# Kernel optimization log

Hardware: AMD Instinct MI355X
Metric: run time of the kernel (lower is better)

Reference implementation:

```python
import jax, jax.numpy as jnp
import numpy as np

N, E, D, F, T, P, C = 100000, 50000, 128, 128, 128, 128, 256


def sparsemax(z):
    """Sparsemax along the last axis (Martins & Astudillo 2016)."""
    K = z.shape[-1]
    zs = -jnp.sort(-z, axis=-1)  # descending
    k = jnp.arange(1, K + 1, dtype=z.dtype)
    zc = jnp.cumsum(zs, axis=-1)
    support = (1.0 + k * zs) > zc
    kz = jnp.sum(support, axis=-1, keepdims=True).astype(z.dtype)
    tau = (jnp.sum(jnp.where(support, zs, 0.0), axis=-1, keepdims=True) - 1.0) / kz
    return jnp.maximum(z - tau, 0.0)


def time_encode(dt, w, b):
    return jnp.cos(dt[:, None] * w[None, :] + b[None, :])


def gru_update(msg, h, W_ih, b_ih, W_hh, b_hh):
    gi = msg @ W_ih.T + b_ih  # [M,3D]
    gh = h @ W_hh.T + b_hh
    r = jax.nn.sigmoid(gi[:, :D] + gh[:, :D])
    z = jax.nn.sigmoid(gi[:, D:2 * D] + gh[:, D:2 * D])
    n = jnp.tanh(gi[:, 2 * D:] + r * gh[:, 2 * D:])
    return (1.0 - z) * n + z * h


def setup_inputs() -> dict:
    key = jax.random.key(0)
    ks = jax.random.split(key, 16)
    s = 0.05
    return {
        'node_memory': jax.random.normal(ks[0], (N, D), jnp.float32),
        'last_update': jax.random.uniform(ks[1], (N,), jnp.float32),
        'node_features': jax.random.normal(ks[2], (N, D), jnp.float32),
        'event_feat': jax.random.normal(ks[3], (E, F), jnp.float32),
        't': jax.random.uniform(ks[4], (E,), jnp.float32) * 10.0,
        'src': jax.random.randint(ks[5], (E,), 0, N),
        'dst': jax.random.randint(ks[6], (E,), 0, N),
        'time_w': jax.random.normal(ks[7], (T,), jnp.float32),
        'time_b': jax.random.normal(ks[8], (T,), jnp.float32),
        'W_ih': jax.random.normal(ks[9], (3 * D, 2 * D + F + T), jnp.float32) * s,
        'b_ih': jnp.zeros((3 * D,), jnp.float32),
        'W_hh': jax.random.normal(ks[10], (3 * D, D), jnp.float32) * s,
        'b_hh': jnp.zeros((3 * D,), jnp.float32),
        'proj_W': jax.random.normal(ks[11], (D, P), jnp.float32) * s,
        'proj_b': jnp.zeros((P,), jnp.float32),
        'centroids': jax.random.normal(ks[12], (C, P), jnp.float32),
    }


def reference(node_memory, last_update, node_features, event_feat, t, src, dst,
              time_w, time_b, W_ih, b_ih, W_hh, b_hh, proj_W, proj_b, centroids):
    # --- store_events: original events + flipped direction (sn + dn stores) ---
    idx = jnp.concatenate([src, dst])            # [2E] destination-of-update node
    other = jnp.concatenate([dst, src])          # [2E]
    tt = jnp.concatenate([t, t])                 # [2E]
    ef = jnp.concatenate([event_feat, event_feat])  # [2E,F]

    # --- message function: concat(self-mem, other-mem, event-feat, time-enc) ---
    dt = tt - last_update[idx]
    msg = jnp.concatenate([node_memory[idx], node_memory[other], ef,
                           time_encode(dt, time_w, time_b)], axis=-1)  # [2E, 2D+F+T]

    # --- message aggregator (mean) + scatter_max of timestamps ---
    msg_sum = jax.ops.segment_sum(msg, idx, num_segments=N)
    cnt = jax.ops.segment_sum(jnp.ones_like(tt), idx, num_segments=N)
    agg = msg_sum / jnp.maximum(cnt, 1.0)[:, None]
    has = cnt > 0
    upd_t = jax.ops.segment_max(tt, idx, num_segments=N)

    # --- memory updater (GRU) applied only where events arrived ---
    upd_memory = gru_update(agg, node_memory, W_ih, b_ih, W_hh, b_hh)
    new_memory = jnp.where(has[:, None], upd_memory, node_memory)  # [N,D]
    new_last = jnp.where(has, jnp.maximum(upd_t, last_update), last_update)

    # --- _detect_communities ---
    feat = new_memory + node_features
    pf = feat @ proj_W + proj_b  # [N,P]
    pf_n = pf / (jnp.linalg.norm(pf, axis=-1, keepdims=True) + 1e-8)
    cen_n = centroids / (jnp.linalg.norm(centroids, axis=-1, keepdims=True) + 1e-8)
    sim = pf_n @ cen_n.T                     # [N,C] cosine similarity
    nc_membership = sparsemax(sim)           # [N,C]
    cn_membership = sparsemax(sim.T)         # [C,N]
    c_memory = cn_membership @ new_memory    # [C,D]
    # community last-update via masked max (scatter_max over nonzero memberships)
    c_t = jnp.max(jnp.where(cn_membership > 0, new_last[None, :], -jnp.inf), axis=1)

    # --- embedder readout: node memory enriched with community memory ---
    emb = new_memory + nc_membership @ c_memory  # [N,D]
    return emb
```

## Files before the change

kernel.cpp:

```cpp
#include <hip/hip_runtime.h>
#include <math.h>

#define N_NODES 100000
#define N_EV    50000
#define CAP     6144
#define MAXE    24

typedef __attribute__((ext_vector_type(8))) short short8;
typedef __attribute__((ext_vector_type(4))) float f32x4;
typedef __attribute__((ext_vector_type(8))) _Float16 half8;

static __device__ __forceinline__ short f2bf(float f) {
    union { float f; unsigned u; } v; v.f = f;
    unsigned r = (v.u + 0x7FFFu + ((v.u >> 16) & 1u)) >> 16;
    return (short)r;
}
static __device__ __forceinline__ float bf2f(short h) {
    union { unsigned u; float f; } v; v.u = ((unsigned)(unsigned short)h) << 16;
    return v.f;
}
static __device__ __forceinline__ float fast_cos(float x) {
    float r = x * 0.15915494309189535f;
    r = r - floorf(r);
    return __builtin_amdgcn_cosf(r);
}
static __device__ __forceinline__ float fast_sigmoid(float x) {
    float e = __builtin_amdgcn_exp2f(-1.4426950408889634f * x);
    return __builtin_amdgcn_rcpf(1.f + e);
}
static __device__ __forceinline__ float fast_tanh(float x) {
    float e = __builtin_amdgcn_exp2f(2.8853900817779268f * x);
    return 1.f - 2.f * __builtin_amdgcn_rcpf(e + 1.f);
}

__global__ void k_build(const float* __restrict__ W_ih, const float* __restrict__ b_ih,
                        const float* __restrict__ W_hh, const float* __restrict__ b_hh,
                        short* __restrict__ Wbf, float* __restrict__ bcat) {
    int idx = blockIdx.x * 256 + threadIdx.x;
    int j = idx & 7, lane = (idx >> 3) & 63, sub = idx >> 9;
    int ks = sub & 15, NB = sub >> 4;
    int k = ks * 32 + ((lane >> 4) & 3) * 8 + j;
    int o = NB * 16 + (lane & 15);
    int g = o >> 7, d = o & 127;
    float v;
    if (g == 0)      v = W_ih[d * 512 + k] + (k < 128 ? W_hh[d * 128 + k] : 0.f);
    else if (g == 1) v = W_ih[(128 + d) * 512 + k] + (k < 128 ? W_hh[(128 + d) * 128 + k] : 0.f);
    else if (g == 2) v = W_ih[(256 + d) * 512 + k];
    else             v = (k < 128 ? W_hh[(256 + d) * 128 + k] : 0.f);
    Wbf[idx] = f2bf(v);
    if (idx < 512) {
        int gg = idx >> 7, dd = idx & 127;
        float b;
        if (gg == 0)      b = b_ih[dd] + b_hh[dd];
        else if (gg == 1) b = b_ih[128 + dd] + b_hh[128 + dd];
        else if (gg == 2) b = b_ih[256 + dd];
        else              b = b_hh[256 + dd];
        bcat[idx] = b;
    }
}

__global__ void k_cen(const float* __restrict__ centroids,
                      short* __restrict__ cenf_hi, short* __restrict__ cenf_lo) {
    int c = blockIdx.x, t = threadIdx.x;
    float v = centroids[c * 128 + t];
    float ss = v * v;
    #pragma unroll
    for (int m = 1; m < 64; m <<= 1) ss += __shfl_xor(ss, m);
    __shared__ float tmp[2];
    if ((t & 63) == 0) tmp[t >> 6] = ss;
    __syncthreads();
    float tot = tmp[0] + tmp[1];
    float nv = v / (sqrtf(tot) + 1e-8f);
    short hi = f2bf(nv);
    short lo = f2bf(nv - bf2f(hi));
    int ct = c >> 4, c_l = c & 15, kstep = t >> 5, kj = t & 31;
    int lane = c_l + 16 * (kj >> 3), j = kj & 7;
    int fidx = ((ct * 4 + kstep) * 64 + lane) * 8 + j;
    cenf_hi[fidx] = hi;
    cenf_lo[fidx] = lo;
}

__global__ void k_packW(const float* __restrict__ proj_W,
                        short* __restrict__ pw_hi, short* __restrict__ pw_lo) {
    int idx = blockIdx.x * 256 + threadIdx.x;
    int k = idx >> 7, p = idx & 127;
    float v = proj_W[k * 128 + p];
    short hi = f2bf(v);
    short lo = f2bf(v - bf2f(hi));
    int pt = p >> 4, p_l = p & 15, kstep = k >> 5, kj = k & 31;
    int lane = p_l + 16 * (kj >> 3), j = kj & 7;
    int fidx = ((pt * 4 + kstep) * 64 + lane) * 8 + j;
    pw_hi[fidx] = hi;
    pw_lo[fidx] = lo;
}

__global__ __launch_bounds__(256) void k_fill(
        const float* __restrict__ t_arr, const int* __restrict__ src,
        const int* __restrict__ dst, int* __restrict__ cnt_i,
        int4* __restrict__ elist) {
    int e = blockIdx.x * 256 + threadIdx.x;
    if (e >= 2 * N_EV) return;
    int eb  = e < N_EV ? e : e - N_EV;
    int idx = e < N_EV ? src[eb] : dst[eb];
    int oth = e < N_EV ? dst[eb] : src[eb];
    float tt = t_arr[eb];
    int p = atomicAdd(&cnt_i[idx], 1);
    if (p < MAXE)
        elist[(size_t)idx * MAXE + p] = make_int4(eb, oth, __float_as_int(tt), 0);
}

__global__ __launch_bounds__(512, 4) void k_gru(
        const float* __restrict__ node_memory, const float* __restrict__ last_update,
        const float* __restrict__ event_feat,
        const float* __restrict__ time_w, const float* __restrict__ time_b,
        const int* __restrict__ cnt_i, const int4* __restrict__ elist,
        const short* __restrict__ Wbf, const float* __restrict__ bcat,
        float* __restrict__ new_mem) {
    __shared__ __align__(16) short Ab[32 * 512];
    int t = threadIdx.x;
    int n0 = blockIdx.x * 32;
    int g = t >> 4, q = t & 15;
    int n = n0 + g;
    int rawc = cnt_i[n];
    int ec = rawc < MAXE ? rawc : MAXE;
    float lu = last_update[n];
    float tw[8], tb[8];
    #pragma unroll
    for (int j = 0; j < 8; j++) { tw[j] = time_w[q * 8 + j]; tb[j] = time_b[q * 8 + j]; }
    float ao[8], af[8], at[8];
    #pragma unroll
    for (int j = 0; j < 8; j++) { ao[j] = 0.f; af[j] = 0.f; at[j] = 0.f; }
    const int4* ep = elist + (size_t)n * MAXE;
    #pragma unroll
    for (int e = 0; e < 4; e++) {
        if (e < ec) {
            int4 ev = ep[e];
            int eb = ev.x, oth = ev.y;
            float dt = __int_as_float(ev.z) - lu;
            const float4* om = (const float4*)&node_memory[(size_t)oth * 128 + q * 8];
            const float4* ef = (const float4*)&event_feat[(size_t)eb * 128 + q * 8];
            float4 o0 = om[0], o1 = om[1];
            float4 f0 = ef[0], f1 = ef[1];
            ao[0] += o0.x; ao[1] += o0.y; ao[2] += o0.z; ao[3] += o0.w;
            ao[4] += o1.x; ao[5] += o1.y; ao[6] += o1.z; ao[7] += o1.w;
            af[0] += f0.x; af[1] += f0.y; af[2] += f0.z; af[3] += f0.w;
            af[4] += f1.x; af[5] += f1.y; af[6] += f1.z; af[7] += f1.w;
            #pragma unroll
            for (int j = 0; j < 8; j++) at[j] += fast_cos(fmaf(dt, tw[j], tb[j]));
        }
    }
    for (int e = 4; e < ec; e++) {
        int4 ev = ep[e];
        int eb = ev.x, oth = ev.y;
        float dt = __int_as_float(ev.z) - lu;
        const float4* om = (const float4*)&node_memory[(size_t)oth * 128 + q * 8];
        const float4* ef = (const float4*)&event_feat[(size_t)eb * 128 + q * 8];
        float4 o0 = om[0], o1 = om[1];
        float4 f0 = ef[0], f1 = ef[1];
        ao[0] += o0.x; ao[1] += o0.y; ao[2] += o0.z; ao[3] += o0.w;
        ao[4] += o1.x; ao[5] += o1.y; ao[6] += o1.z; ao[7] += o1.w;
        af[0] += f0.x; af[1] += f0.y; af[2] += f0.z; af[3] += f0.w;
        af[4] += f1.x; af[5] += f1.y; af[6] += f1.z; af[7] += f1.w;
        #pragma unroll
        for (int j = 0; j < 8; j++) at[j] += fast_cos(fmaf(dt, tw[j], tb[j]));
    }
    float inv = 1.f / fmaxf((float)rawc, 1.f);
    #pragma unroll
    for (int pass = 0; pass < 4; pass++) {
        float vals[8];
        if (pass == 0) {
            const float4* p = (const float4*)&node_memory[(size_t)n * 128 + q * 8];
            float4 x = p[0], y = p[1];
            vals[0]=x.x; vals[1]=x.y; vals[2]=x.z; vals[3]=x.w;
            vals[4]=y.x; vals[5]=y.y; vals[6]=y.z; vals[7]=y.w;
        } else if (pass == 1) {
            #pragma unroll
            for (int j = 0; j < 8; j++) vals[j] = ao[j] * inv;
        } else if (pass == 2) {
            #pragma unroll
            for (int j = 0; j < 8; j++) vals[j] = af[j] * inv;
        } else {
            #pragma unroll
            for (int j = 0; j < 8; j++) vals[j] = at[j] * inv;
        }
        int k0 = q * 8 + pass * 128;
        int mb = g >> 4, ks = k0 >> 5;
        int lane = ((k0 >> 3) & 3) * 16 + (g & 15);
        int gi = (mb * 16 + ks) * 64 + lane;
        gi ^= ((gi >> 4) & 7);
        short8 sv;
        #pragma unroll
        for (int j = 0; j < 8; j++) sv[j] = f2bf(vals[j]);
        *(short8*)&Ab[gi * 8] = sv;
    }
    __syncthreads();

    int w = t >> 6, l = t & 63;
    f32x4 acc[2][4];
    #pragma unroll
    for (int mb = 0; mb < 2; mb++)
        #pragma unroll
        for (int gg = 0; gg < 4; gg++) acc[mb][gg] = (f32x4){0.f, 0.f, 0.f, 0.f};

    const short8* Bp = (const short8*)Wbf;
    #pragma unroll 4
    for (int ks = 0; ks < 16; ks++) {
        short8 afr[2];
        #pragma unroll
        for (int mb = 0; mb < 2; mb++) {
            int gi = (mb * 16 + ks) * 64 + l;
            gi ^= ((gi >> 4) & 7);
            afr[mb] = *(const short8*)&Ab[gi * 8];
        }
        #pragma unroll
        for (int gate = 0; gate < 4; gate++) {
            short8 bfr = Bp[(((w + 8 * gate) * 16 + ks) * 64) + l];
            acc[0][gate] = __builtin_amdgcn_mfma_f32_16x16x32_bf16(afr[0], bfr, acc[0][gate], 0, 0, 0);
            acc[1][gate] = __builtin_amdgcn_mfma_f32_16x16x32_bf16(afr[1], bfr, acc[1][gate], 0, 0, 0);
        }
    }

    int c_l = l & 15, rq = l >> 4;
    int d = w * 16 + c_l;
    float br = bcat[d], bz = bcat[128 + d], bn = bcat[256 + d], bh = bcat[384 + d];
    #pragma unroll
    for (int mb = 0; mb < 2; mb++)
        #pragma unroll
        for (int r = 0; r < 4; r++) {
            int nn = n0 + mb * 16 + rq * 4 + r;
            int cn = cnt_i[nn];
            float h = node_memory[(size_t)nn * 128 + d];
            float rs = acc[mb][0][r] + br;
            float zs = acc[mb][1][r] + bz;
            float gn = acc[mb][2][r] + bn;
            float gh = acc[mb][3][r] + bh;
            float r_ = fast_sigmoid(rs);
            float z_ = fast_sigmoid(zs);
            float nn2 = fast_tanh(gn + r_ * gh);
            float nm = (1.f - z_) * nn2 + z_ * h;
            new_mem[(size_t)nn * 128 + d] = (cn > 0) ? nm : h;
        }
}

__global__ __launch_bounds__(256, 2) void k_sim(
        const float* __restrict__ new_mem, const float* __restrict__ node_features,
        const short* __restrict__ pw_hi, const short* __restrict__ pw_lo,
        const float* __restrict__ proj_b,
        const short* __restrict__ cenf_hi, const short* __restrict__ cenf_lo,
        _Float16* __restrict__ simT) {
    __shared__ __align__(16) float feat[64 * 128];
    __shared__ __align__(16) short pfh[64 * 128];
    __shared__ __align__(16) short pfl[64 * 128];
    int t = threadIdx.x;
    int n0 = blockIdx.x * 64;

    #pragma unroll
    for (int r = 0; r < 8; r++) {
        int idx = r * 256 + t;
        int node = idx >> 5, gk = idx & 31;
        float4 v = make_float4(0.f, 0.f, 0.f, 0.f);
        int n = n0 + node;
        if (n < N_NODES) {
            float4 a = *(const float4*)&new_mem[(size_t)n * 128 + gk * 4];
            float4 b = *(const float4*)&node_features[(size_t)n * 128 + gk * 4];
            v = make_float4(a.x + b.x, a.y + b.y, a.z + b.z, a.w + b.w);
        }
        int gs = gk ^ (node & 7);
        *(float4*)&feat[(node * 32 + gs) * 4] = v;
    }
    __syncthreads();

    int w = t >> 6, l = t & 63;
    int lm = l & 15, lk = l >> 4;

    f32x4 pacc[8];
    #pragma unroll
    for (int nb = 0; nb < 8; nb++) pacc[nb] = (f32x4){0.f, 0.f, 0.f, 0.f};
    #pragma unroll
    for (int ks = 0; ks < 4; ks++) {
        int node = w * 16 + lm;
        int gk0 = ks * 8 + lk * 2;
        float4 a0 = *(const float4*)&feat[(node * 32 + (gk0 ^ (node & 7))) * 4];
        float4 a1 = *(const float4*)&feat[(node * 32 + ((gk0 + 1) ^ (node & 7))) * 4];
        float av[8] = {a0.x, a0.y, a0.z, a0.w, a1.x, a1.y, a1.z, a1.w};
        short8 Ah, Al;
        #pragma unroll
        for (int j = 0; j < 8; j++) {
            short h = f2bf(av[j]);
            Ah[j] = h;
            Al[j] = f2bf(av[j] - bf2f(h));
        }
        #pragma unroll
        for (int nb = 0; nb < 8; nb++) {
            int fidx = ((nb * 4 + ks) * 64 + l) * 8;
            short8 Bh = *(const short8*)&pw_hi[fidx];
            short8 Bl = *(const short8*)&pw_lo[fidx];
            pacc[nb] = __builtin_amdgcn_mfma_f32_16x16x32_bf16(Ah, Bh, pacc[nb], 0, 0, 0);
            pacc[nb] = __builtin_amdgcn_mfma_f32_16x16x32_bf16(Ah, Bl, pacc[nb], 0, 0, 0);
            pacc[nb] = __builtin_amdgcn_mfma_f32_16x16x32_bf16(Al, Bh, pacc[nb], 0, 0, 0);
        }
    }
    float ssq[4] = {0.f, 0.f, 0.f, 0.f};
    #pragma unroll
    for (int nb = 0; nb < 8; nb++) {
        float pb = proj_b[nb * 16 + lm];
        #pragma unroll
        for (int r = 0; r < 4; r++) {
            pacc[nb][r] += pb;
            ssq[r] = fmaf(pacc[nb][r], pacc[nb][r], ssq[r]);
        }
    }
    #pragma unroll
    for (int m = 1; m < 16; m <<= 1)
        #pragma unroll
        for (int r = 0; r < 4; r++) ssq[r] += __shfl_xor(ssq[r], m);
    float inv[4];
    #pragma unroll
    for (int r = 0; r < 4; r++) inv[r] = 1.f / (sqrtf(ssq[r]) + 1e-8f);
    #pragma unroll
    for (int nb = 0; nb < 8; nb++)
        #pragma unroll
        for (int r = 0; r < 4; r++) {
            float v = pacc[nb][r] * inv[r];
            short h = f2bf(v);
            short lo2 = f2bf(v - bf2f(h));
            int node = w * 16 + lk * 4 + r;
            int p = nb * 16 + lm;
            int g = node * 16 + (((p >> 3)) ^ (node & 7));
            int si = g * 8 + (p & 7);
            pfh[si] = h;
            pfl[si] = lo2;
        }
    __syncthreads();

    f32x4 sacc[4][4];
    #pragma unroll
    for (int ct = 0; ct < 4; ct++)
        #pragma unroll
        for (int mt = 0; mt < 4; mt++) sacc[ct][mt] = (f32x4){0.f, 0.f, 0.f, 0.f};
    #pragma unroll
    for (int ks = 0; ks < 4; ks++) {
        short8 Bh[4], Bl[4];
        #pragma unroll
        for (int mt = 0; mt < 4; mt++) {
            int node = mt * 16 + lm;
            int g = node * 16 + ((ks * 4 + lk) ^ (node & 7));
            Bh[mt] = *(const short8*)&pfh[g * 8];
            Bl[mt] = *(const short8*)&pfl[g * 8];
        }
        #pragma unroll
        for (int ct = 0; ct < 4; ct++) {
            int ctg = w * 4 + ct;
            int fidx = ((ctg * 4 + ks) * 64 + l) * 8;
            short8 Ah = *(const short8*)&cenf_hi[fidx];
            short8 Al = *(const short8*)&cenf_lo[fidx];
            #pragma unroll
            for (int mt = 0; mt < 4; mt++) {
                sacc[ct][mt] = __builtin_amdgcn_mfma_f32_16x16x32_bf16(Ah, Bh[mt], sacc[ct][mt], 0, 0, 0);
                sacc[ct][mt] = __builtin_amdgcn_mfma_f32_16x16x32_bf16(Ah, Bl[mt], sacc[ct][mt], 0, 0, 0);
                sacc[ct][mt] = __builtin_amdgcn_mfma_f32_16x16x32_bf16(Al, Bh[mt], sacc[ct][mt], 0, 0, 0);
            }
        }
    }
    #pragma unroll
    for (int ct = 0; ct < 4; ct++) {
        int cbase = (w * 4 + ct) * 16 + lk * 4;
        #pragma unroll
        for (int r = 0; r < 4; r++) {
            size_t rowoff = (size_t)(cbase + r) * N_NODES;
            #pragma unroll
            for (int mt = 0; mt < 4; mt++) {
                int n = n0 + mt * 16 + lm;
                if (n < N_NODES) simT[rowoff + n] = (_Float16)sacc[ct][mt][r];
            }
        }
    }
}

static __device__ float tau_eval(const float* __restrict__ g, int cid, float lo, float w) {
    float K[32], S[32];
    #pragma unroll
    for (int j = 0; j < 32; j++)
        K[j] = g[cid * 128 + j] + g[cid * 128 + 32 + j] + g[cid * 128 + 64 + j] + g[cid * 128 + 96 + j];
    float acc = 0.f;
    for (int b = 31; b >= 0; b--) {
        float Kn = (b == 31) ? 0.f : K[b + 1];
        acc += (K[b] - Kn) * (lo + b * w);
        S[b] = acc;
    }
    float tau = (S[0] - 1.f) / fmaxf(K[0], 1.f);
    float best = tau;
    int jprev = -1;
    for (int it = 0; it < 48; it++) {
        int j = (int)floorf((tau - lo) / w);
        j = j < 0 ? 0 : (j > 31 ? 31 : j);
        if (j > 0 && lo + j * w > tau) j--;
        float Kj = K[j];
        if (Kj < 0.5f) break;
        float tn = (S[j] - 1.f) / Kj;
        if (tn > best) best = tn;
        if (j == jprev) break;
        jprev = j;
        tau = tn;
    }
    return best;
}

template <int LVL>
__global__ __launch_bounds__(256) void k_lad(const _Float16* __restrict__ simT,
                                             const float* __restrict__ g0,
                                             float* __restrict__ gout) {
    constexpr float W = (LVL == 0) ? 0.0625f : 0.008f;
    int cid = blockIdx.x >> 2, slice = blockIdx.x & 3;
    int t = threadIdx.x, l = t & 63, wv = t >> 6;
    __shared__ float lo_s;
    if (t == 0) {
        float lo = -1.03125f;
        if (LVL == 1) lo = tau_eval(g0, cid, -1.03125f, 0.0625f);
        lo_s = lo;
    }
    __syncthreads();
    float lo = lo_s;
    const half8* z8 = (const half8*)(simT + (size_t)cid * N_NODES);
    int cnt[32];
    #pragma unroll
    for (int j = 0; j < 32; j++) cnt[j] = 0;
    int base0 = slice * 3125, end = base0 + 3125;
    for (int base = base0; base < end; base += 256) {
        int i = base + t;
        float b[8];
        #pragma unroll
        for (int j = 0; j < 8; j++) b[j] = -3.f;
        if (i < end) {
            half8 a = z8[i];
            #pragma unroll
            for (int j = 0; j < 8; j++) b[j] = (float)a[j] - lo;
        }
        #pragma unroll
        for (int j = 0; j < 32; j++) {
            float T = j * W;
            int c0 = __popcll(__ballot(b[0] > T)) + __popcll(__ballot(b[1] > T))
                   + __popcll(__ballot(b[2] > T)) + __popcll(__ballot(b[3] > T));
            int c1 = __popcll(__ballot(b[4] > T)) + __popcll(__ballot(b[5] > T))
                   + __popcll(__ballot(b[6] > T)) + __popcll(__ballot(b[7] > T));
            cnt[j] += c0 + c1;
        }
    }
    __shared__ int red[4][32];
    if (l == 0) {
        #pragma unroll
        for (int j = 0; j < 32; j++) red[wv][j] = cnt[j];
    }
    __syncthreads();
    if (t < 32) {
        float v = (float)(red[0][t] + red[1][t] + red[2][t] + red[3][t]);
        gout[cid * 128 + slice * 32 + t] = v;
    }
}

__global__ __launch_bounds__(256) void k_gather(const _Float16* __restrict__ simT,
                                                const float* __restrict__ g0,
                                                const float* __restrict__ g1,
                                                int* __restrict__ ccount,
                                                float2* __restrict__ clist) {
    int cid = blockIdx.x >> 2, slice = blockIdx.x & 3;
    __shared__ float th_s;
    if (threadIdx.x == 0) {
        float t1 = tau_eval(g0, cid, -1.03125f, 0.0625f);
        th_s = tau_eval(g1, cid, t1, 0.008f) - 1e-5f;
    }
    __syncthreads();
    float th = th_s;
    const half8* z8 = (const half8*)(simT + (size_t)cid * N_NODES);
    int t = threadIdx.x;
    int end = slice * 3125 + 3125;
    for (int i = slice * 3125 + t; i < end; i += 256) {
        half8 a = z8[i];
        int nb = i * 8;
        #pragma unroll
        for (int j = 0; j < 8; j++) {
            float v = (float)a[j];
            if (v > th) {
                int p = atomicAdd(&ccount[cid], 1);
                if (p < CAP) clist[(size_t)cid * CAP + p] = make_float2(v, __int_as_float(nb + j));
            }
        }
    }
}

__global__ __launch_bounds__(256) void k_csolve(
        const _Float16* __restrict__ simT, const float* __restrict__ new_mem,
        const int* __restrict__ ccount, const float2* __restrict__ clist,
        float* __restrict__ c_mem) {
    int c = blockIdx.x, t = threadIdx.x;
    __shared__ float zv[CAP];
    __shared__ int   zn[CAP];
    __shared__ float redS[4], redK[4], part[256];
    int raw = ccount[c];
    if (raw == 0) {
        if (t < 128) c_mem[c * 128 + t] = 0.f;
        return;
    }
    float tau;
    if (raw <= CAP) {
        int cnt = raw;
        for (int i = t; i < cnt; i += 256) {
            float2 e = clist[(size_t)c * CAP + i];
            zv[i] = e.x; zn[i] = __float_as_int(e.y);
        }
        __syncthreads();
        float ls = 0.f;
        for (int i = t; i < cnt; i += 256) ls += zv[i];
        #pragma unroll
        for (int m = 1; m < 64; m <<= 1) ls += __shfl_xor(ls, m);
        if ((t & 63) == 0) redS[t >> 6] = ls;
        __syncthreads();
        tau = (redS[0] + redS[1] + redS[2] + redS[3] - 1.f) / (float)cnt;
        float kprev = (float)cnt;
        for (int it = 0; it < 64; it++) {
            float s = 0.f, k = 0.f;
            for (int i = t; i < cnt; i += 256) {
                float v = zv[i];
                if (v > tau) { s += v; k += 1.f; }
            }
            #pragma unroll
            for (int m = 1; m < 64; m <<= 1) { s += __shfl_xor(s, m); k += __shfl_xor(k, m); }
            __syncthreads();
            if ((t & 63) == 0) { redS[t >> 6] = s; redK[t >> 6] = k; }
            __syncthreads();
            float S_ = redS[0] + redS[1] + redS[2] + redS[3];
            float K_ = redK[0] + redK[1] + redK[2] + redK[3];
            if (K_ == kprev || K_ < 0.5f) break;
            kprev = K_;
            tau = (S_ - 1.f) / K_;
        }
        int d = t & 127, half = t >> 7;
        float acc = 0.f;
        for (int i = half; i < cnt; i += 2) {
            float w = zv[i] - tau;
            if (w > 0.f) acc = fmaf(w, new_mem[(size_t)zn[i] * 128 + d], acc);
        }
        part[t] = acc;
        __syncthreads();
        if (t < 128) c_mem[c * 128 + t] = part[t] + part[t + 128];
    } else {
        const _Float16* z = simT + (size_t)c * N_NODES;
        float ls = 0.f;
        for (int n = t; n < N_NODES; n += 256) ls += (float)z[n];
        #pragma unroll
        for (int m = 1; m < 64; m <<= 1) ls += __shfl_xor(ls, m);
        if ((t & 63) == 0) redS[t >> 6] = ls;
        __syncthreads();
        tau = (redS[0] + redS[1] + redS[2] + redS[3] - 1.f) / (float)N_NODES;
        float kprev = -1.f;
        for (int it = 0; it < 64; it++) {
            float s = 0.f, k = 0.f;
            for (int n = t; n < N_NODES; n += 256) {
                float v = (float)z[n];
                if (v > tau) { s += v; k += 1.f; }
            }
            #pragma unroll
            for (int m = 1; m < 64; m <<= 1) { s += __shfl_xor(s, m); k += __shfl_xor(k, m); }
            __syncthreads();
            if ((t & 63) == 0) { redS[t >> 6] = s; redK[t >> 6] = k; }
            __syncthreads();
            float S_ = redS[0] + redS[1] + redS[2] + redS[3];
            float K_ = redK[0] + redK[1] + redK[2] + redK[3];
            if (K_ == kprev || K_ < 0.5f) break;
            kprev = K_;
            tau = (S_ - 1.f) / K_;
        }
        int d = t & 127, half = t >> 7;
        float acc = 0.f;
        for (int n = half; n < N_NODES; n += 2) {
            float w = (float)z[n] - tau;
            if (w > 0.f) acc = fmaf(w, new_mem[(size_t)n * 128 + d], acc);
        }
        part[t] = acc;
        __syncthreads();
        if (t < 128) c_mem[c * 128 + t] = part[t] + part[t + 128];
    }
}

__global__ __launch_bounds__(512) void k_emb(
        const _Float16* __restrict__ simT, const float* __restrict__ c_mem,
        float* __restrict__ out) {
    __shared__ float zb[32 * 257];
    __shared__ float2 suppl[32][64];
    __shared__ int suppc[32];
    int t = threadIdx.x;
    int n0 = blockIdx.x * 32;
    #pragma unroll
    for (int r = 0; r < 2; r++) {
        int idx = r * 512 + t;
        int c = idx >> 2, nq = idx & 3;
        half8 v = *(const half8*)&simT[(size_t)c * N_NODES + n0 + nq * 8];
        #pragma unroll
        for (int j = 0; j < 8; j++) zb[(nq * 8 + j) * 257 + c] = (float)v[j];
    }
    __syncthreads();
    int n_l = t >> 4, g = t & 15;
    const float* zr = zb + n_l * 257;
    float zv[16];
    #pragma unroll
    for (int j = 0; j < 16; j++) zv[j] = zr[g + 16 * j];
    float s = 0.f;
    #pragma unroll
    for (int j = 0; j < 16; j++) s += zv[j];
    #pragma unroll
    for (int m = 1; m < 16; m <<= 1) s += __shfl_xor(s, m);
    float tau = (s - 1.f) / 256.f;
    float kprev = -1.f;
    for (int it = 0; it < 40; it++) {
        float ls = 0.f, lk = 0.f;
        #pragma unroll
        for (int j = 0; j < 16; j++) {
            float v = zv[j];
            if (v > tau) { ls += v; lk += 1.f; }
        }
        #pragma unroll
        for (int m = 1; m < 16; m <<= 1) { ls += __shfl_xor(ls, m); lk += __shfl_xor(lk, m); }
        if (lk == kprev) break;
        kprev = lk;
        tau = (ls - 1.f) / lk;
    }
    int gw = (t >> 4) & 3;
    int base = 0;
    #pragma unroll
    for (int j = 0; j < 16; j++) {
        float m = zv[j] - tau;
        bool pred = m > 0.f;
        unsigned long long mask = __ballot(pred);
        unsigned gm = (unsigned)((mask >> (gw * 16)) & 0xFFFFull);
        if (pred) {
            int idx = base + __popc(gm & ((1u << g) - 1u));
            if (idx < 64) suppl[n_l][idx] = make_float2(m, __int_as_float(g + 16 * j));
        }
        base += __popc(gm);
    }
    if (g == 0) suppc[n_l] = base;
    __syncthreads();
    float acc[8];
    #pragma unroll
    for (int j = 0; j < 8; j++) acc[j] = 0.f;
    int cnt_s = suppc[n_l];
    if (cnt_s <= 64) {
        for (int i = 0; i < cnt_s; i++) {
            float2 e = suppl[n_l][i];
            int c = __float_as_int(e.y);
            const float* cm = c_mem + c * 128 + g * 8;
            #pragma unroll
            for (int j = 0; j < 8; j++) acc[j] = fmaf(e.x, cm[j], acc[j]);
        }
    } else {
        for (int c = 0; c < 256; c++) {
            float m = zr[c] - tau;
            if (m > 0.f) {
                const float* cm = c_mem + c * 128 + g * 8;
                #pragma unroll
                for (int j = 0; j < 8; j++) acc[j] = fmaf(m, cm[j], acc[j]);
            }
        }
    }
    float* op = out + (size_t)(n0 + n_l) * 128 + g * 8;
    #pragma unroll
    for (int j = 0; j < 8; j++) op[j] += acc[j];
}

extern "C" void kernel_launch(void* const* d_in, const int* in_sizes, int n_in,
                              void* d_out, int out_size, void* d_ws, size_t ws_size,
                              hipStream_t stream) {
    const float* node_memory   = (const float*)d_in[0];
    const float* last_update   = (const float*)d_in[1];
    const float* node_features = (const float*)d_in[2];
    const float* event_feat    = (const float*)d_in[3];
    const float* t_arr         = (const float*)d_in[4];
    const int*   src           = (const int*)d_in[5];
    const int*   dst           = (const int*)d_in[6];
    const float* time_w        = (const float*)d_in[7];
    const float* time_b        = (const float*)d_in[8];
    const float* W_ih          = (const float*)d_in[9];
    const float* b_ih          = (const float*)d_in[10];
    const float* W_hh          = (const float*)d_in[11];
    const float* b_hh          = (const float*)d_in[12];
    const float* proj_W        = (const float*)d_in[13];
    const float* proj_b        = (const float*)d_in[14];
    const float* centroids     = (const float*)d_in[15];

    char* wsb      = (char*)d_ws;
    _Float16* simT = (_Float16*)wsb;
    int*   cnt_i  = (int*)(wsb + (size_t)256 * N_NODES * 2);
    int4*  elist  = (int4*)(cnt_i + N_NODES);
    short* Wbf    = (short*)(elist + (size_t)N_NODES * MAXE);
    float* bcat   = (float*)(Wbf + 512 * 512);
    float* c_mem  = bcat + 512;
    float* gc0    = c_mem + 32768;
    float* gc1    = gc0 + 32768;
    int*   ccount = (int*)(gc1 + 32768);
    float2* clist = (float2*)(ccount + 256);
    short* cenf_hi = (short*)(clist + (size_t)256 * CAP);
    short* cenf_lo = cenf_hi + 256 * 128;
    short* pw_hi   = cenf_lo + 256 * 128;
    short* pw_lo   = pw_hi + 128 * 128;
    float* out    = (float*)d_out;

    hipMemsetAsync(cnt_i, 0, N_NODES * sizeof(int), stream);
    hipMemsetAsync(ccount, 0, 256 * sizeof(int), stream);
    k_build<<<1024, 256, 0, stream>>>(W_ih, b_ih, W_hh, b_hh, Wbf, bcat);
    k_cen<<<256, 128, 0, stream>>>(centroids, cenf_hi, cenf_lo);
    k_packW<<<64, 256, 0, stream>>>(proj_W, pw_hi, pw_lo);
    k_fill<<<(2 * N_EV + 255) / 256, 256, 0, stream>>>(t_arr, src, dst, cnt_i, elist);
    k_gru<<<N_NODES / 32, 512, 0, stream>>>(node_memory, last_update, event_feat,
                                            time_w, time_b, cnt_i, elist, Wbf, bcat, out);
    k_sim<<<(N_NODES + 63) / 64, 256, 0, stream>>>(out, node_features, pw_hi, pw_lo,
                                                   proj_b, cenf_hi, cenf_lo, simT);
    k_lad<0><<<1024, 256, 0, stream>>>(simT, nullptr, gc0);
    k_lad<1><<<1024, 256, 0, stream>>>(simT, gc0, gc1);
    k_gather<<<1024, 256, 0, stream>>>(simT, gc0, gc1, ccount, clist);
    k_csolve<<<256, 256, 0, stream>>>(simT, out, ccount, clist, c_mem);
    k_emb<<<N_NODES / 32, 512, 0, stream>>>(simT, c_mem, out);
}
```

Measured before the change: 483.7 us.

## Fuse column-sparsemax ladder, gather and solve into one per-community kernel

Replaces the four kernels (two histogram ladder passes, gather, and csolve) with a single k_comm kernel that runs one 512-thread block per community. The histograms are reduced and tau evaluated in shared memory, and candidates are compacted straight into LDS using wave-aggregated atomics instead of global per-element atomics and a global clist. This removes three launches, the global round-trips for histograms and candidate lists, and a memset. The cost is that only 256 blocks cover the three 200KB row scans instead of 1024, which may underuse the GPU's bandwidth.

Measured after the change: 489.7 us. About the same (+1.2%).

```diff
diff --git a/kernel.cpp b/kernel.cpp
--- a/kernel.cpp
+++ b/kernel.cpp
@@ -377,11 +377,8 @@
     }
 }
 
-static __device__ float tau_eval(const float* __restrict__ g, int cid, float lo, float w) {
-    float K[32], S[32];
-    #pragma unroll
-    for (int j = 0; j < 32; j++)
-        K[j] = g[cid * 128 + j] + g[cid * 128 + 32 + j] + g[cid * 128 + 64 + j] + g[cid * 128 + 96 + j];
+static __device__ float tau_eval_local(const float* __restrict__ K, float lo, float w) {
+    float S[32];
     float acc = 0.f;
     for (int b = 31; b >= 0; b--) {
         float Kn = (b == 31) ? 0.f : K[b + 1];
@@ -406,179 +403,176 @@
     return best;
 }
 
-template <int LVL>
-__global__ __launch_bounds__(256) void k_lad(const _Float16* __restrict__ simT,
-                                             const float* __restrict__ g0,
-                                             float* __restrict__ gout) {
-    constexpr float W = (LVL == 0) ? 0.0625f : 0.008f;
-    int cid = blockIdx.x >> 2, slice = blockIdx.x & 3;
-    int t = threadIdx.x, l = t & 63, wv = t >> 6;
-    __shared__ float lo_s;
-    if (t == 0) {
-        float lo = -1.03125f;
-        if (LVL == 1) lo = tau_eval(g0, cid, -1.03125f, 0.0625f);
-        lo_s = lo;
-    }
-    __syncthreads();
-    float lo = lo_s;
-    const half8* z8 = (const half8*)(simT + (size_t)cid * N_NODES);
-    int cnt[32];
-    #pragma unroll
-    for (int j = 0; j < 32; j++) cnt[j] = 0;
-    int base0 = slice * 3125, end = base0 + 3125;
-    for (int base = base0; base < end; base += 256) {
-        int i = base + t;
-        float b[8];
-        #pragma unroll
-        for (int j = 0; j < 8; j++) b[j] = -3.f;
-        if (i < end) {
-            half8 a = z8[i];
-            #pragma unroll
-            for (int j = 0; j < 8; j++) b[j] = (float)a[j] - lo;
-        }
-        #pragma unroll
-        for (int j = 0; j < 32; j++) {
-            float T = j * W;
-            int c0 = __popcll(__ballot(b[0] > T)) + __popcll(__ballot(b[1] > T))
-                   + __popcll(__ballot(b[2] > T)) + __popcll(__ballot(b[3] > T));
-            int c1 = __popcll(__ballot(b[4] > T)) + __popcll(__ballot(b[5] > T))
-                   + __popcll(__ballot(b[6] > T)) + __popcll(__ballot(b[7] > T));
-            cnt[j] += c0 + c1;
-        }
-    }
-    __shared__ int red[4][32];
-    if (l == 0) {
-        #pragma unroll
-        for (int j = 0; j < 32; j++) red[wv][j] = cnt[j];
-    }
-    __syncthreads();
-    if (t < 32) {
-        float v = (float)(red[0][t] + red[1][t] + red[2][t] + red[3][t]);
-        gout[cid * 128 + slice * 32 + t] = v;
-    }
-}
-
-__global__ __launch_bounds__(256) void k_gather(const _Float16* __restrict__ simT,
-                                                const float* __restrict__ g0,
-                                                const float* __restrict__ g1,
-                                                int* __restrict__ ccount,
-                                                float2* __restrict__ clist) {
-    int cid = blockIdx.x >> 2, slice = blockIdx.x & 3;
-    __shared__ float th_s;
-    if (threadIdx.x == 0) {
-        float t1 = tau_eval(g0, cid, -1.03125f, 0.0625f);
-        th_s = tau_eval(g1, cid, t1, 0.008f) - 1e-5f;
-    }
-    __syncthreads();
-    float th = th_s;
-    const half8* z8 = (const half8*)(simT + (size_t)cid * N_NODES);
-    int t = threadIdx.x;
-    int end = slice * 3125 + 3125;
-    for (int i = slice * 3125 + t; i < end; i += 256) {
-        half8 a = z8[i];
-        int nb = i * 8;
-        #pragma unroll
-        for (int j = 0; j < 8; j++) {
-            float v = (float)a[j];
-            if (v > th) {
-                int p = atomicAdd(&ccount[cid], 1);
-                if (p < CAP) clist[(size_t)cid * CAP + p] = make_float2(v, __int_as_float(nb + j));
-            }
-        }
-    }
-}
-
-__global__ __launch_bounds__(256) void k_csolve(
+__global__ __launch_bounds__(512) void k_comm(
         const _Float16* __restrict__ simT, const float* __restrict__ new_mem,
-        const int* __restrict__ ccount, const float2* __restrict__ clist,
         float* __restrict__ c_mem) {
-    int c = blockIdx.x, t = threadIdx.x;
+    int c = blockIdx.x, t = threadIdx.x, l = t & 63, wv = t >> 6;
+    const half8* z8 = (const half8*)(simT + (size_t)c * N_NODES);
+    __shared__ int red[8][32];
+    __shared__ float Klds[32];
+    __shared__ float lo_s, th_s;
+    __shared__ int cnt_s;
     __shared__ float zv[CAP];
     __shared__ int   zn[CAP];
-    __shared__ float redS[4], redK[4], part[256];
-    int raw = ccount[c];
+    __shared__ float redS[8], redK[8], part[512];
+
+    #pragma unroll
+    for (int LVL = 0; LVL < 2; LVL++) {
+        float W = (LVL == 0) ? 0.0625f : 0.008f;
+        float lo = (LVL == 0) ? -1.03125f : lo_s;
+        int cnt[32];
+        #pragma unroll
+        for (int j = 0; j < 32; j++) cnt[j] = 0;
+        for (int i = t; i < 12500; i += 512) {
+            half8 a = z8[i];
+            float b[8];
+            #pragma unroll
+            for (int j = 0; j < 8; j++) b[j] = (float)a[j] - lo;
+            #pragma unroll
+            for (int j = 0; j < 32; j++) {
+                float T = j * W;
+                int c0 = __popcll(__ballot(b[0] > T)) + __popcll(__ballot(b[1] > T))
+                       + __popcll(__ballot(b[2] > T)) + __popcll(__ballot(b[3] > T));
+                int c1 = __popcll(__ballot(b[4] > T)) + __popcll(__ballot(b[5] > T))
+                       + __popcll(__ballot(b[6] > T)) + __popcll(__ballot(b[7] > T));
+                cnt[j] += c0 + c1;
+            }
+        }
+        if (l == 0) {
+            #pragma unroll
+            for (int j = 0; j < 32; j++) red[wv][j] = cnt[j];
+        }
+        __syncthreads();
+        if (t < 32) {
+            int s = 0;
+            #pragma unroll
+            for (int w2 = 0; w2 < 8; w2++) s += red[w2][t];
+            Klds[t] = (float)s;
+        }
+        __syncthreads();
+        if (t == 0) {
+            float tv = tau_eval_local(Klds, lo, W);
+            if (LVL == 0) lo_s = tv;
+            else          th_s = tv - 1e-5f;
+            cnt_s = 0;
+        }
+        __syncthreads();
+    }
+
+    float th = th_s;
+    for (int base = 0; base < 12500; base += 512) {
+        int i = base + t;
+        half8 a;
+        bool valid = i < 12500;
+        if (valid) a = z8[i];
+        #pragma unroll
+        for (int j = 0; j < 8; j++) {
+            float v = valid ? (float)a[j] : -3.f;
+            bool p = v > th;
+            unsigned long long mask = __ballot(p);
+            int wcount = __popcll(mask);
+            int base_w = 0;
+            if (wcount > 0) {
+                if (l == 0) base_w = atomicAdd(&cnt_s, wcount);
+                base_w = __shfl(base_w, 0);
+                if (p) {
+                    int idx = base_w + __popcll(mask & ((1ull << l) - 1ull));
+                    if (idx < CAP) { zv[idx] = v; zn[idx] = i * 8 + j; }
+                }
+            }
+        }
+    }
+    __syncthreads();
+    int raw = cnt_s;
+    float tau;
     if (raw == 0) {
         if (t < 128) c_mem[c * 128 + t] = 0.f;
         return;
     }
-    float tau;
     if (raw <= CAP) {
         int cnt = raw;
-        for (int i = t; i < cnt; i += 256) {
-            float2 e = clist[(size_t)c * CAP + i];
-            zv[i] = e.x; zn[i] = __float_as_int(e.y);
-        }
+        float ls = 0.f;
+        for (int i = t; i < cnt; i += 512) ls += zv[i];
+        #pragma unroll
+        for (int m = 1; m < 64; m <<= 1) ls += __shfl_xor(ls, m);
+        if (l == 0) redS[wv] = ls;
         __syncthreads();
-        float ls = 0.f;
-        for (int i = t; i < cnt; i += 256) ls += zv[i];
-        #pragma unroll
-        for (int m = 1; m < 64; m <<= 1) ls += __shfl_xor(ls, m);
-        if ((t & 63) == 0) redS[t >> 6] = ls;
-        __syncthreads();
-        tau = (redS[0] + redS[1] + redS[2] + redS[3] - 1.f) / (float)cnt;
+        {
+            float S_ = 0.f;
+            #pragma unroll
+            for (int w2 = 0; w2 < 8; w2++) S_ += redS[w2];
+            tau = (S_ - 1.f) / (float)cnt;
+        }
         float kprev = (float)cnt;
         for (int it = 0; it < 64; it++) {
             float s = 0.f, k = 0.f;
-            for (int i = t; i < cnt; i += 256) {
+            for (int i = t; i < cnt; i += 512) {
                 float v = zv[i];
                 if (v > tau) { s += v; k += 1.f; }
             }
             #pragma unroll
             for (int m = 1; m < 64; m <<= 1) { s += __shfl_xor(s, m); k += __shfl_xor(k, m); }
             __syncthreads();
-            if ((t & 63) == 0) { redS[t >> 6] = s; redK[t >> 6] = k; }
+            if (l == 0) { redS[wv] = s; redK[wv] = k; }
             __syncthreads();
-            float S_ = redS[0] + redS[1] + redS[2] + redS[3];
-            float K_ = redK[0] + redK[1] + redK[2] + redK[3];
+            float S_ = 0.f, K_ = 0.f;
+            #pragma unroll
+            for (int w2 = 0; w2 < 8; w2++) { S_ += redS[w2]; K_ += redK[w2]; }
             if (K_ == kprev || K_ < 0.5f) break;
             kprev = K_;
             tau = (S_ - 1.f) / K_;
         }
-        int d = t & 127, half = t >> 7;
+        int d = t & 127, qq = t >> 7;
         float acc = 0.f;
-        for (int i = half; i < cnt; i += 2) {
+        for (int i = qq; i < cnt; i += 4) {
             float w = zv[i] - tau;
             if (w > 0.f) acc = fmaf(w, new_mem[(size_t)zn[i] * 128 + d], acc);
         }
         part[t] = acc;
         __syncthreads();
-        if (t < 128) c_mem[c * 128 + t] = part[t] + part[t + 128];
+        if (t < 128) c_mem[c * 128 + t] = part[t] + part[t + 128] + part[t + 256] + part[t + 384];
     } else {
         const _Float16* z = simT + (size_t)c * N_NODES;
         float ls = 0.f;
-        for (int n = t; n < N_NODES; n += 256) ls += (float)z[n];
+        for (int n = t; n < N_NODES; n += 512) ls += (float)z[n];
         #pragma unroll
         for (int m = 1; m < 64; m <<= 1) ls += __shfl_xor(ls, m);
-        if ((t & 63) == 0) redS[t >> 6] = ls;
+        if (l == 0) redS[wv] = ls;
         __syncthreads();
-        tau = (redS[0] + redS[1] + redS[2] + redS[3] - 1.f) / (float)N_NODES;
+        {
+            float S_ = 0.f;
+            #pragma unroll
+            for (int w2 = 0; w2 < 8; w2++) S_ += redS[w2];
+            tau = (S_ - 1.f) / (float)N_NODES;
+        }
         float kprev = -1.f;
         for (int it = 0; it < 64; it++) {
             float s = 0.f, k = 0.f;
-            for (int n = t; n < N_NODES; n += 256) {
+            for (int n = t; n < N_NODES; n += 512) {
                 float v = (float)z[n];
                 if (v > tau) { s += v; k += 1.f; }
             }
             #pragma unroll
             for (int m = 1; m < 64; m <<= 1) { s += __shfl_xor(s, m); k += __shfl_xor(k, m); }
             __syncthreads();
-            if ((t & 63) == 0) { redS[t >> 6] = s; redK[t >> 6] = k; }
+            if (l == 0) { redS[wv] = s; redK[wv] = k; }
             __syncthreads();
-            float S_ = redS[0] + redS[1] + redS[2] + redS[3];
-            float K_ = redK[0] + redK[1] + redK[2] + redK[3];
+            float S_ = 0.f, K_ = 0.f;
+            #pragma unroll
+            for (int w2 = 0; w2 < 8; w2++) { S_ += redS[w2]; K_ += redK[w2]; }
             if (K_ == kprev || K_ < 0.5f) break;
             kprev = K_;
             tau = (S_ - 1.f) / K_;
         }
-        int d = t & 127, half = t >> 7;
+        int d = t & 127, qq = t >> 7;
         float acc = 0.f;
-        for (int n = half; n < N_NODES; n += 2) {
+        for (int n = qq; n < N_NODES; n += 4) {
             float w = (float)z[n] - tau;
             if (w > 0.f) acc = fmaf(w, new_mem[(size_t)n * 128 + d], acc);
         }
         part[t] = acc;
         __syncthreads();
-        if (t < 128) c_mem[c * 128 + t] = part[t] + part[t + 128];
+        if (t < 128) c_mem[c * 128 + t] = part[t] + part[t + 128] + part[t + 256] + part[t + 384];
     }
 }
 
@@ -694,18 +688,13 @@
     short* Wbf    = (short*)(elist + (size_t)N_NODES * MAXE);
     float* bcat   = (float*)(Wbf + 512 * 512);
     float* c_mem  = bcat + 512;
-    float* gc0    = c_mem + 32768;
-    float* gc1    = gc0 + 32768;
-    int*   ccount = (int*)(gc1 + 32768);
-    float2* clist = (float2*)(ccount + 256);
-    short* cenf_hi = (short*)(clist + (size_t)256 * CAP);
+    short* cenf_hi = (short*)(c_mem + 32768);
     short* cenf_lo = cenf_hi + 256 * 128;
     short* pw_hi   = cenf_lo + 256 * 128;
     short* pw_lo   = pw_hi + 128 * 128;
     float* out    = (float*)d_out;
 
     hipMemsetAsync(cnt_i, 0, N_NODES * sizeof(int), stream);
-    hipMemsetAsync(ccount, 0, 256 * sizeof(int), stream);
     k_build<<<1024, 256, 0, stream>>>(W_ih, b_ih, W_hh, b_hh, Wbf, bcat);
     k_cen<<<256, 128, 0, stream>>>(centroids, cenf_hi, cenf_lo);
     k_packW<<<64, 256, 0, stream>>>(proj_W, pw_hi, pw_lo);
@@ -714,9 +703,6 @@
                                             time_w, time_b, cnt_i, elist, Wbf, bcat, out);
     k_sim<<<(N_NODES + 63) / 64, 256, 0, stream>>>(out, node_features, pw_hi, pw_lo,
                                                    proj_b, cenf_hi, cenf_lo, simT);
-    k_lad<0><<<1024, 256, 0, stream>>>(simT, nullptr, gc0);
-    k_lad<1><<<1024, 256, 0, stream>>>(simT, gc0, gc1);
-    k_gather<<<1024, 256, 0, stream>>>(simT, gc0, gc1, ccount, clist);
-    k_csolve<<<256, 256, 0, stream>>>(simT, out, ccount, clist, c_mem);
+    k_comm<<<256, 512, 0, stream>>>(simT, out, c_mem);
     k_emb<<<N_NODES / 32, 512, 0, stream>>>(simT, c_mem, out);
 }
```
